# Kernel optimization log

Measured on AMD Instinct MI355X. Metric: run time of the kernel, lower is better.

The kernel has to match this reference:

```python
import jax, jax.numpy as jnp
import numpy as np

B, N, F, DEG = 64, 1024, 128, 8
K1, K2, K3 = 512, 256, 128  # ceil(0.5*N) cascaded pool sizes
NUM_CLASSES = 10
E = B * N * DEG

def _elu(x):
    return jnp.where(x > 0, x, jnp.expm1(x))

def gcn(x, W, b, src, dst, ev, n):
    # PyG GCNConv with improved=True: self-loop weight 2, symmetric norm
    h = x @ W
    w = ev.astype(h.dtype)
    deg = jax.ops.segment_sum(w, dst, num_segments=n) + 2.0
    dinv = jax.lax.rsqrt(deg)
    coef = (w * dinv[src] * dinv[dst])[:, None]
    out = jax.ops.segment_sum(h[src] * coef, dst, num_segments=n)
    out = out + h * (2.0 * dinv * dinv)[:, None]  # self-loop term
    return out + b

def topk_pool(x, p, src, dst, ev, bg, npg, k):
    # score = tanh(x.p/||p||); keep top-k per graph; mask+remap edges
    score = jnp.tanh((x @ p) / jnp.linalg.norm(p))
    vals, idx = jax.lax.top_k(score.reshape(bg, npg), k)
    perm = (idx + (jnp.arange(bg) * npg)[:, None]).reshape(-1)
    x_new = x[perm] * vals.reshape(-1)[:, None]
    remap = jnp.full((bg * npg,), -1, jnp.int32).at[perm].set(
        jnp.arange(bg * k, dtype=jnp.int32))
    s2, d2 = remap[src], remap[dst]
    ev2 = ev & (s2 >= 0) & (d2 >= 0)
    return x_new, jnp.maximum(s2, 0), jnp.maximum(d2, 0), ev2, perm

def setup_inputs() -> dict:
    key = jax.random.key(0)
    ks = jax.random.split(key, 16)
    offs = (jnp.arange(B) * N)[:, None]
    e_per = DEG * N
    src = (jax.random.randint(ks[0], (B, e_per), 0, N) + offs).reshape(-1).astype(jnp.int32)
    dst = (jax.random.randint(ks[1], (B, e_per), 0, N) + offs).reshape(-1).astype(jnp.int32)
    def w(k, shape, fan_in):
        return jax.random.normal(k, shape, jnp.float32) / np.sqrt(fan_in)
    return {
        "x": jax.random.normal(ks[2], (B * N, F), jnp.float32),
        "W1": w(ks[3], (F, 32), F), "b1": jnp.zeros((32,)), "p1": w(ks[4], (32,), 32),
        "W2": w(ks[5], (32, 64), 32), "b2": jnp.zeros((64,)), "p2": w(ks[6], (64,), 64),
        "W3": w(ks[7], (64, 128), 64), "b3": jnp.zeros((128,)), "p3": w(ks[8], (128,), 128),
        "W4": w(ks[9], (128, 256), 128), "b4": jnp.zeros((256,)),
        "W5": w(ks[10], (384, 128), 384), "b5": jnp.zeros((128,)),
        "W6": w(ks[11], (192, 64), 192), "b6": jnp.zeros((64,)),
        "W7": w(ks[12], (96, 32), 96), "b7": jnp.zeros((32,)),
        "Wl": w(ks[13], (64, 64), 64),
        "Wc": w(ks[14], (64, NUM_CLASSES), 64), "bc": jnp.zeros((NUM_CLASSES,)),
        "src": src, "dst": dst,
    }

def reference(x, W1, b1, p1, W2, b2, p2, W3, b3, p3, W4, b4,
              W5, b5, W6, b6, W7, b7, Wl, Wc, bc, src, dst):
    ev0 = jnp.ones((E,), bool)
    x1 = _elu(gcn(x, W1, b1, src, dst, ev0, B * N))
    x2, s2, d2, ev2, idx2 = topk_pool(x1, p1, src, dst, ev0, B, N, K1)
    x2 = _elu(x2)
    x3 = _elu(gcn(x2, W2, b2, s2, d2, ev2, B * K1))
    x4, s4, d4, ev4, idx4 = topk_pool(x3, p2, s2, d2, ev2, B, K1, K2)
    x4 = _elu(x4)
    x5 = _elu(gcn(x4, W3, b3, s4, d4, ev4, B * K2))
    x6, s6, d6, ev6, idx6 = topk_pool(x5, p3, s4, d4, ev4, B, K2, K3)
    x6 = _elu(x6)
    x7 = _elu(gcn(x6, W4, b4, s6, d6, ev6, B * K3))
    x8 = jnp.zeros((B * K2, 256), x7.dtype).at[idx6].set(x7)
    x8 = _elu(jnp.concatenate([x8, x5], axis=1))
    x9 = _elu(gcn(x8, W5, b5, s4, d4, ev4, B * K2))
    x10 = jnp.zeros((B * K1, 128), x9.dtype).at[idx4].set(x9)
    x10 = _elu(jnp.concatenate([x10, x3], axis=1))
    x11 = _elu(gcn(x10, W6, b6, s2, d2, ev2, B * K1))
    x12 = jnp.zeros((B * N, 64), x11.dtype).at[idx2].set(x11)
    x12 = _elu(jnp.concatenate([x12, x1], axis=1))
    x13 = _elu(gcn(x12, W7, b7, src, dst, ev0, B * N))
    batch = jnp.repeat(jnp.arange(B), N)
    gmp = jax.ops.segment_max(x13, batch, num_segments=B)
    gap = jax.ops.segment_sum(x13, batch, num_segments=B) / N
    g = _elu(jnp.concatenate([gmp, gap], axis=1))
    g = _elu(g @ Wl)
    logits = g @ Wc + bc
    return jax.nn.log_softmax(logits, axis=-1)
```

## Files before the change

kernel.cpp:

```cpp
#include <hip/hip_runtime.h>
#include <hip/hip_bf16.h>
#include <math.h>

#define B_ 64
#define N_ 1024
#define E_ 524288
#define K1_ 512
#define K2_ 256
#define K3_ 128
#define M0_ 65536
#define M1_ 32768
#define M2_ 16384
#define M3_ 8192

static __device__ __forceinline__ float eluf(float x){ return x > 0.f ? x : expm1f(x); }
static __device__ __forceinline__ float4 elu4(float4 v){
  float4 o; o.x=eluf(v.x); o.y=eluf(v.y); o.z=eluf(v.z); o.w=eluf(v.w); return o;
}

template<int BM,int BN,int MODE>
__global__ __launch_bounds__(256) void k_mm(const float* __restrict__ X,
    const float* __restrict__ W, float* __restrict__ H, int M, int K, int N,
    const int* __restrict__ perm, const float* __restrict__ vals,
    const float* __restrict__ Xd, const int* __restrict__ orig,
    const int* __restrict__ rm, int WD4){
  constexpr int TX = BN/4;
  constexpr int TY = 256/TX;
  constexpr int RM = BM/TY;
  __shared__ float Xs[BM][36];
  __shared__ float Ws[32][BN];
  const int t = threadIdx.x;
  const int tx = t % TX, ty = t / TX;
  const int m0 = blockIdx.x*BM, n0 = blockIdx.y*BN;
  float acc[RM][4];
  #pragma unroll
  for (int r=0;r<RM;++r){acc[r][0]=0.f;acc[r][1]=0.f;acc[r][2]=0.f;acc[r][3]=0.f;}
  for (int k0=0;k0<K;k0+=32){
    #pragma unroll
    for (int r=0;r<BM/32;++r){
      int fi=r*256+t, row=fi>>3, q=fi&7;
      int m = m0+row;
      int c4 = (k0>>2)+q;
      float4 v;
      if (MODE==0){
        v = *(const float4*)(X + (size_t)m*K + (c4<<2));
      } else if (MODE==1){
        int pm = perm[m]; float vv = vals[m];
        float4 h = *(const float4*)(X + (size_t)pm*K + (c4<<2));
        v.x=eluf(h.x*vv); v.y=eluf(h.y*vv); v.z=eluf(h.z*vv); v.w=eluf(h.w*vv);
      } else {
        if (c4 < WD4){
          int o = orig ? orig[m] : m;
          int j = rm[o];
          if (j>=0) v = elu4(*(const float4*)(Xd + ((size_t)j*WD4 + c4)*4));
          else { v.x=0.f;v.y=0.f;v.z=0.f;v.w=0.f; }
        } else {
          int ws4 = (K>>2) - WD4;
          v = elu4(*(const float4*)(X + ((size_t)m*ws4 + (c4-WD4))*4));
        }
      }
      *(float4*)(&Xs[row][q*4]) = v;
    }
    #pragma unroll
    for (int r=0;r<BN/32;++r){
      int fi=r*256+t, row=fi/(BN/4), q=fi%(BN/4);
      *(float4*)(&Ws[row][q*4]) = *(const float4*)(W + (size_t)(k0+row)*N + n0 + q*4);
    }
    __syncthreads();
    #pragma unroll
    for (int kk=0;kk<32;++kk){
      float4 wv = *(const float4*)(&Ws[kk][tx*4]);
      #pragma unroll
      for (int r=0;r<RM;++r){
        float xv = Xs[ty*RM+r][kk];
        acc[r][0]=fmaf(xv,wv.x,acc[r][0]);
        acc[r][1]=fmaf(xv,wv.y,acc[r][1]);
        acc[r][2]=fmaf(xv,wv.z,acc[r][2]);
        acc[r][3]=fmaf(xv,wv.w,acc[r][3]);
      }
    }
    __syncthreads();
  }
  #pragma unroll
  for (int r=0;r<RM;++r){
    int m = m0 + ty*RM + r;
    float4 h; h.x=acc[r][0];h.y=acc[r][1];h.z=acc[r][2];h.w=acc[r][3];
    *(float4*)(H + (size_t)m*N + n0 + tx*4) = h;
  }
}

__global__ void k_deg0(const int* __restrict__ dst, int* __restrict__ degi){
  int i = blockIdx.x*256+threadIdx.x; if (i>=E_) return;
  atomicAdd(&degi[dst[i]], 1);
}
__global__ void k_place0(const int* __restrict__ src, const int* __restrict__ dst,
                         int* __restrict__ cursor, int* __restrict__ col){
  int i = blockIdx.x*256+threadIdx.x; if (i>=E_) return;
  int p = atomicAdd(&cursor[dst[i]], 1);
  col[p] = src[i];
}

__global__ __launch_bounds__(256) void k_scanA(const int* __restrict__ degi,
                                               int* __restrict__ bsum){
  __shared__ int ls[256];
  int b = blockIdx.x, t = threadIdx.x;
  ls[t] = degi[b*256+t]; __syncthreads();
  for (int o=128;o>0;o>>=1){ if (t<o) ls[t]+=ls[t+o]; __syncthreads(); }
  if (t==0) bsum[b] = ls[0];
}
__global__ __launch_bounds__(256) void k_scanB(int* __restrict__ bsum){
  __shared__ int ps[256];
  int t = threadIdx.x;
  ps[t] = bsum[t]; __syncthreads();
  for (int o=1;o<256;o<<=1){
    int v = (t>=o) ? ps[t-o] : 0;
    __syncthreads(); ps[t]+=v; __syncthreads();
  }
  bsum[t] = ps[t];
}
__global__ __launch_bounds__(256) void k_scanC(const int* __restrict__ degi,
    const int* __restrict__ bsum, int* __restrict__ rowptr,
    int* __restrict__ cursor, float* __restrict__ dinv){
  __shared__ int ps[256];
  int b = blockIdx.x, t = threadIdx.x;
  int i = b*256+t;
  int d = degi[i];
  ps[t] = d; __syncthreads();
  for (int o=1;o<256;o<<=1){
    int v = (t>=o) ? ps[t-o] : 0;
    __syncthreads(); ps[t]+=v; __syncthreads();
  }
  int off = (b==0 ? 0 : bsum[b-1]) + ps[t] - d;
  rowptr[i] = off; cursor[i] = off;
  dinv[i] = rsqrtf((float)d + 2.f);
  if (i == M0_-1) rowptr[M0_] = off + d;
}

__global__ void k_deg_orig(const int* __restrict__ orig, const int* __restrict__ rowptr0,
                           const int* __restrict__ col0, const int* __restrict__ rm,
                           float* __restrict__ dinv, int M){
  int i = blockIdx.x*256+threadIdx.x; if (i>=M) return;
  int o = orig[i];
  int beg = rowptr0[o], end = rowptr0[o+1];
  int d = 0;
  for (int j=beg;j<end;++j) d += (rm[col0[j]] >= 0) ? 1 : 0;
  dinv[i] = rsqrtf((float)d + 2.f);
}

__global__ void k_compose_idx(const int* __restrict__ prevOrig, const int* __restrict__ idxL,
                              int* __restrict__ origL, int n){
  int i = blockIdx.x*256+threadIdx.x; if (i<n) origL[i] = prevOrig[idxL[i]];
}

template<int F, bool SCORE>
__global__ __launch_bounds__(256) void k_gather(const int* __restrict__ rowptr,
    const int* __restrict__ col, const float* __restrict__ dinv,
    const float* __restrict__ H, const float* __restrict__ bias,
    float* __restrict__ OUT, int M,
    const float* __restrict__ p, float* __restrict__ score){
  constexpr int FQ = F/4;
  int i = blockIdx.x*256+threadIdx.x;
  if (i >= M*FQ) return;
  int n = i/FQ, q = i - (i/FQ)*FQ;
  int beg = rowptr[n], end = rowptr[n+1];
  float4 acc; acc.x=0.f;acc.y=0.f;acc.z=0.f;acc.w=0.f;
  for (int j=beg;j<end;++j){
    int s = col[j];
    float c = dinv[s];
    float4 h = *(const float4*)(H + (size_t)s*F + q*4);
    acc.x=fmaf(c,h.x,acc.x); acc.y=fmaf(c,h.y,acc.y);
    acc.z=fmaf(c,h.z,acc.z); acc.w=fmaf(c,h.w,acc.w);
  }
  float dn = dinv[n];
  float sc = 2.f*dn*dn;
  float4 hn = *(const float4*)(H + (size_t)n*F + q*4);
  float4 bv = *(const float4*)(bias + q*4);
  float4 o;
  o.x = eluf(fmaf(sc,hn.x,fmaf(dn,acc.x,bv.x)));
  o.y = eluf(fmaf(sc,hn.y,fmaf(dn,acc.y,bv.y)));
  o.z = eluf(fmaf(sc,hn.z,fmaf(dn,acc.z,bv.z)));
  o.w = eluf(fmaf(sc,hn.w,fmaf(dn,acc.w,bv.w)));
  *(float4*)(OUT + (size_t)n*F + q*4) = o;
  if (SCORE){
    float4 pv = *(const float4*)(p + q*4);
    float dot = o.x*pv.x + o.y*pv.y + o.z*pv.z + o.w*pv.w;
    float n2  = pv.x*pv.x + pv.y*pv.y + pv.z*pv.z + pv.w*pv.w;
    #pragma unroll
    for (int mk=FQ>>1; mk>0; mk>>=1){
      dot += __shfl_xor(dot, mk);
      n2  += __shfl_xor(n2,  mk);
    }
    if (q==0) score[n] = tanhf(dot * rsqrtf(n2));
  }
}

template<int F, bool SCORE>
__global__ __launch_bounds__(256) void k_gather_rm(const int* __restrict__ orig,
    const int* __restrict__ rowptr0, const int* __restrict__ col0,
    const int* __restrict__ rm, const float* __restrict__ dinv,
    const float* __restrict__ H, const float* __restrict__ bias,
    float* __restrict__ OUT, int M,
    const float* __restrict__ p, float* __restrict__ score){
  constexpr int FQ = F/4;
  int i = blockIdx.x*256+threadIdx.x;
  if (i >= M*FQ) return;
  int n = i/FQ, q = i - (i/FQ)*FQ;
  int o = orig[n];
  int beg = rowptr0[o], end = rowptr0[o+1];
  float4 acc; acc.x=0.f;acc.y=0.f;acc.z=0.f;acc.w=0.f;
  for (int j=beg;j<end;++j){
    int s = rm[col0[j]];
    if (s >= 0){
      float c = dinv[s];
      float4 h = *(const float4*)(H + (size_t)s*F + q*4);
      acc.x=fmaf(c,h.x,acc.x); acc.y=fmaf(c,h.y,acc.y);
      acc.z=fmaf(c,h.z,acc.z); acc.w=fmaf(c,h.w,acc.w);
    }
  }
  float dn = dinv[n];
  float sc = 2.f*dn*dn;
  float4 hn = *(const float4*)(H + (size_t)n*F + q*4);
  float4 bv = *(const float4*)(bias + q*4);
  float4 ov;
  ov.x = eluf(fmaf(sc,hn.x,fmaf(dn,acc.x,bv.x)));
  ov.y = eluf(fmaf(sc,hn.y,fmaf(dn,acc.y,bv.y)));
  ov.z = eluf(fmaf(sc,hn.z,fmaf(dn,acc.z,bv.z)));
  ov.w = eluf(fmaf(sc,hn.w,fmaf(dn,acc.w,bv.w)));
  *(float4*)(OUT + (size_t)n*F + q*4) = ov;
  if (SCORE){
    float4 pv = *(const float4*)(p + q*4);
    float dot = ov.x*pv.x + ov.y*pv.y + ov.z*pv.z + ov.w*pv.w;
    float n2  = pv.x*pv.x + pv.y*pv.y + pv.z*pv.z + pv.w*pv.w;
    #pragma unroll
    for (int mk=FQ>>1; mk>0; mk>>=1){
      dot += __shfl_xor(dot, mk);
      n2  += __shfl_xor(n2,  mk);
    }
    if (q==0) score[n] = tanhf(dot * rsqrtf(n2));
  }
}

__global__ void k_topk(const float* __restrict__ score, int npg, int K,
                       int* __restrict__ perm, float* __restrict__ vals){
  __shared__ float ss[1024]; __shared__ int si[1024];
  int g = blockIdx.x, tid = threadIdx.x;
  ss[tid] = score[g*npg + tid]; si[tid] = tid;
  __syncthreads();
  for (int k=2;k<=npg;k<<=1){
    for (int j=k>>1;j>0;j>>=1){
      int ixj = tid ^ j;
      if (ixj > tid){
        float s1=ss[tid], s2=ss[ixj]; int i1=si[tid], i2=si[ixj];
        bool aAfterB = (s1 < s2) || (s1==s2 && i1 > i2);
        bool sw = ((tid & k)==0) ? aAfterB : !aAfterB;
        if (sw){ ss[tid]=s2; si[tid]=i2; ss[ixj]=s1; si[ixj]=i1; }
      }
      __syncthreads();
    }
  }
  if (tid < K){ perm[g*K+tid] = g*npg + si[tid]; vals[g*K+tid] = ss[tid]; }
}

__global__ void k_remap_set(const int* __restrict__ perm, int* __restrict__ remap, int n){
  int i = blockIdx.x*256+threadIdx.x; if (i<n) remap[perm[i]] = i;
}

__global__ void k_head(const float* __restrict__ x13, const float* __restrict__ Wl,
                       const float* __restrict__ Wc, const float* __restrict__ bc,
                       float* __restrict__ out){
  __shared__ float smax[256], ssum[256];
  __shared__ float gv[64], g2[64], logit[10];
  int g = blockIdx.x, t = threadIdx.x;
  int f = t & 31, r0 = t >> 5;
  float mx = -3.4e38f, sm = 0.f;
  const float* base = x13 + (size_t)g*N_*32;
  for (int r=r0; r<N_; r+=8){ float v = base[r*32+f]; mx = fmaxf(mx,v); sm += v; }
  smax[t]=mx; ssum[t]=sm; __syncthreads();
  if (t<128){ smax[t]=fmaxf(smax[t],smax[t+128]); ssum[t]+=ssum[t+128]; } __syncthreads();
  if (t<64){ smax[t]=fmaxf(smax[t],smax[t+64]); ssum[t]+=ssum[t+64]; } __syncthreads();
  if (t<32){
    float m2 = fmaxf(smax[t],smax[t+32]); float s2 = ssum[t]+ssum[t+32];
    gv[t] = eluf(m2); gv[32+t] = eluf(s2 * (1.f/N_));
  }
  __syncthreads();
  if (t<64){
    float acc=0.f;
    #pragma unroll
    for (int i2=0;i2<64;++i2) acc = fmaf(gv[i2], Wl[i2*64+t], acc);
    g2[t] = eluf(acc);
  }
  __syncthreads();
  if (t<10){
    float acc = bc[t];
    #pragma unroll
    for (int j=0;j<64;++j) acc = fmaf(g2[j], Wc[j*10+t], acc);
    logit[t] = acc;
  }
  __syncthreads();
  if (t==0){
    float m=-3.4e38f; for (int c=0;c<10;++c) m=fmaxf(m,logit[c]);
    float s=0.f; for (int c=0;c<10;++c) s += expf(logit[c]-m);
    float lse = m + logf(s);
    for (int c=0;c<10;++c) out[g*10+c] = logit[c]-lse;
  }
}

extern "C" void kernel_launch(void* const* d_in, const int* in_sizes, int n_in,
                              void* d_out, int out_size, void* d_ws, size_t ws_size,
                              hipStream_t stream){
  const float* x  = (const float*)d_in[0];
  const float* W1 = (const float*)d_in[1];
  const float* b1 = (const float*)d_in[2];
  const float* p1 = (const float*)d_in[3];
  const float* W2 = (const float*)d_in[4];
  const float* b2 = (const float*)d_in[5];
  const float* p2 = (const float*)d_in[6];
  const float* W3 = (const float*)d_in[7];
  const float* b3 = (const float*)d_in[8];
  const float* p3 = (const float*)d_in[9];
  const float* W4 = (const float*)d_in[10];
  const float* b4 = (const float*)d_in[11];
  const float* W5 = (const float*)d_in[12];
  const float* b5 = (const float*)d_in[13];
  const float* W6 = (const float*)d_in[14];
  const float* b6 = (const float*)d_in[15];
  const float* W7 = (const float*)d_in[16];
  const float* b7 = (const float*)d_in[17];
  const float* Wl = (const float*)d_in[18];
  const float* Wc = (const float*)d_in[19];
  const float* bc = (const float*)d_in[20];
  const int* src0 = (const int*)d_in[21];
  const int* dst0 = (const int*)d_in[22];
  float* out = (float*)d_out;

  char* wsp = (char*)d_ws;
  size_t off = 0;
  auto alloc = [&](size_t bytes)->char*{
    char* p = wsp + off;
    off += (bytes + 255) & ~(size_t)255;
    return p;
  };
  float* bufA = (float*)alloc((size_t)2097152*4);
  float* bufB = (float*)alloc((size_t)2097152*4);
  float* bufC = (float*)alloc((size_t)2097152*4);
  float* bufD = (float*)alloc((size_t)2097152*4);
  float* bufH = (float*)alloc((size_t)2097152*4);
  float* score= (float*)alloc((size_t)M0_*4);
  float* vals2= (float*)alloc((size_t)M1_*4);
  float* vals4= (float*)alloc((size_t)M2_*4);
  float* vals6= (float*)alloc((size_t)M3_*4);
  int* idx2 = (int*)alloc((size_t)M1_*4);
  int* idx4 = (int*)alloc((size_t)M2_*4);
  int* idx6 = (int*)alloc((size_t)M3_*4);
  int* orig4 = (int*)alloc((size_t)M2_*4);
  int* orig6 = (int*)alloc((size_t)M3_*4);
  int* rm02 = (int*)alloc((size_t)M0_*4);
  int* rm04 = (int*)alloc((size_t)M0_*4);
  int* rm06 = (int*)alloc((size_t)M0_*4);
  int* col0 = (int*)alloc((size_t)E_*4);
  int* rowptr0 = (int*)alloc((size_t)(M0_+1)*4);
  int* cursor0 = (int*)alloc((size_t)M0_*4);
  int* degi0 = (int*)alloc((size_t)M0_*4);
  int* bsum  = (int*)alloc((size_t)256*4);
  float* dinv0 = (float*)alloc((size_t)M0_*4);
  float* dinv2 = (float*)alloc((size_t)M1_*4);
  float* dinv4 = (float*)alloc((size_t)M2_*4);
  float* dinv6 = (float*)alloc((size_t)M3_*4);

  auto NB = [](int total){ return (total+255)/256; };

  hipMemsetAsync(degi0, 0, (size_t)M0_*4, stream);
  k_deg0<<<NB(E_),256,0,stream>>>(dst0, degi0);
  k_scanA<<<256,256,0,stream>>>(degi0, bsum);
  k_scanB<<<1,256,0,stream>>>(bsum);
  k_scanC<<<256,256,0,stream>>>(degi0, bsum, rowptr0, cursor0, dinv0);
  k_place0<<<NB(E_),256,0,stream>>>(src0, dst0, cursor0, col0);

  k_mm<64,32,0><<<dim3(M0_/64,1),256,0,stream>>>(x, W1, bufH, M0_, 128, 32,
      nullptr,nullptr,nullptr,nullptr,nullptr,0);
  k_gather<32,true><<<NB(M0_*8),256,0,stream>>>(rowptr0, col0, dinv0, bufH, b1, bufA, M0_, p1, score);

  k_topk<<<B_,1024,0,stream>>>(score, 1024, K1_, idx2, vals2);
  hipMemsetAsync(rm02, 0xFF, (size_t)M0_*4, stream);
  k_remap_set<<<NB(M1_),256,0,stream>>>(idx2, rm02, M1_);
  k_deg_orig<<<NB(M1_),256,0,stream>>>(idx2, rowptr0, col0, rm02, dinv2, M1_);

  k_mm<64,64,1><<<dim3(M1_/64,1),256,0,stream>>>(bufA, W2, bufH, M1_, 32, 64,
      idx2, vals2, nullptr,nullptr,nullptr,0);
  k_gather_rm<64,true><<<NB(M1_*16),256,0,stream>>>(idx2, rowptr0, col0, rm02, dinv2, bufH, b2, bufB, M1_, p2, score);

  k_topk<<<B_,512,0,stream>>>(score, 512, K2_, idx4, vals4);
  k_compose_idx<<<NB(M2_),256,0,stream>>>(idx2, idx4, orig4, M2_);
  hipMemsetAsync(rm04, 0xFF, (size_t)M0_*4, stream);
  k_remap_set<<<NB(M2_),256,0,stream>>>(orig4, rm04, M2_);
  k_deg_orig<<<NB(M2_),256,0,stream>>>(orig4, rowptr0, col0, rm04, dinv4, M2_);

  k_mm<64,64,1><<<dim3(M2_/64,2),256,0,stream>>>(bufB, W3, bufH, M2_, 64, 128,
      idx4, vals4, nullptr,nullptr,nullptr,0);
  k_gather_rm<128,true><<<NB(M2_*32),256,0,stream>>>(orig4, rowptr0, col0, rm04, dinv4, bufH, b3, bufC, M2_, p3, score);

  k_topk<<<B_,256,0,stream>>>(score, 256, K3_, idx6, vals6);
  k_compose_idx<<<NB(M3_),256,0,stream>>>(orig4, idx6, orig6, M3_);
  hipMemsetAsync(rm06, 0xFF, (size_t)M0_*4, stream);
  k_remap_set<<<NB(M3_),256,0,stream>>>(orig6, rm06, M3_);
  k_deg_orig<<<NB(M3_),256,0,stream>>>(orig6, rowptr0, col0, rm06, dinv6, M3_);

  k_mm<64,64,1><<<dim3(M3_/64,4),256,0,stream>>>(bufC, W4, bufH, M3_, 128, 256,
      idx6, vals6, nullptr,nullptr,nullptr,0);
  k_gather_rm<256,false><<<NB(M3_*64),256,0,stream>>>(orig6, rowptr0, col0, rm06, dinv6, bufH, b4, bufD, M3_, nullptr, nullptr);

  k_mm<64,64,2><<<dim3(M2_/64,2),256,0,stream>>>(bufC, W5, bufH, M2_, 384, 128,
      nullptr,nullptr, bufD, orig4, rm06, 64);
  k_gather_rm<128,false><<<NB(M2_*32),256,0,stream>>>(orig4, rowptr0, col0, rm04, dinv4, bufH, b5, bufD, M2_, nullptr, nullptr);

  k_mm<64,64,2><<<dim3(M1_/64,1),256,0,stream>>>(bufB, W6, bufH, M1_, 192, 64,
      nullptr,nullptr, bufD, idx2, rm04, 32);
  k_gather_rm<64,false><<<NB(M1_*16),256,0,stream>>>(idx2, rowptr0, col0, rm02, dinv2, bufH, b6, bufC, M1_, nullptr, nullptr);

  k_mm<64,32,2><<<dim3(M0_/64,1),256,0,stream>>>(bufA, W7, bufH, M0_, 96, 32,
      nullptr,nullptr, bufC, nullptr, rm02, 16);
  k_gather<32,false><<<NB(M0_*8),256,0,stream>>>(rowptr0, col0, dinv0, bufH, b7, bufA, M0_, nullptr, nullptr);

  k_head<<<B_,256,0,stream>>>(bufA, Wl, Wc, bc, out);

  (void)in_sizes; (void)n_in; (void)out_size; (void)ws_size;
}
```

Before: 399.9 us.

## Prefetch next GEMM tile into registers and transpose X tile in shared memory

The tiled GEMM now loads the next K-slice of X and W into registers while computing on the current shared-memory tile, overlapping global loads with FMAs. The X tile is stored transposed in shared memory, so each thread reads its four rows with a single float4 load and the inner loop is hand-unrolled for exactly four rows. The two BN=32 launches move to BM=128 so that every instantiation has four rows per thread. This adds register pressure and relies on RM always being 4, and the transposed scalar stores into shared memory may cause bank conflicts.

After: 416.0 us. 4.0% more time.

```diff
diff --git a/kernel.cpp b/kernel.cpp
--- a/kernel.cpp
+++ b/kernel.cpp
@@ -27,18 +27,23 @@
   constexpr int TX = BN/4;
   constexpr int TY = 256/TX;
   constexpr int RM = BM/TY;
-  __shared__ float Xs[BM][36];
+  constexpr int XLD = BM/32;
+  constexpr int WLD = BN/32;
+  constexpr int XST = BM+4;
+  __shared__ float Xs[32][XST];
   __shared__ float Ws[32][BN];
   const int t = threadIdx.x;
   const int tx = t % TX, ty = t / TX;
   const int m0 = blockIdx.x*BM, n0 = blockIdx.y*BN;
+  float4 xr[XLD], wr[WLD];
   float acc[RM][4];
   #pragma unroll
   for (int r=0;r<RM;++r){acc[r][0]=0.f;acc[r][1]=0.f;acc[r][2]=0.f;acc[r][3]=0.f;}
-  for (int k0=0;k0<K;k0+=32){
-    #pragma unroll
-    for (int r=0;r<BM/32;++r){
-      int fi=r*256+t, row=fi>>3, q=fi&7;
+
+  auto load_step = [&](int k0){
+    #pragma unroll
+    for (int l=0;l<XLD;++l){
+      int fi=l*256+t, row=fi>>3, q=fi&7;
       int m = m0+row;
       int c4 = (k0>>2)+q;
       float4 v;
@@ -59,25 +64,42 @@
           v = elu4(*(const float4*)(X + ((size_t)m*ws4 + (c4-WD4))*4));
         }
       }
-      *(float4*)(&Xs[row][q*4]) = v;
-    }
-    #pragma unroll
-    for (int r=0;r<BN/32;++r){
-      int fi=r*256+t, row=fi/(BN/4), q=fi%(BN/4);
-      *(float4*)(&Ws[row][q*4]) = *(const float4*)(W + (size_t)(k0+row)*N + n0 + q*4);
+      xr[l]=v;
+    }
+    #pragma unroll
+    for (int l=0;l<WLD;++l){
+      int fi=l*256+t, wrow=fi/(BN/4), wq=fi%(BN/4);
+      wr[l] = *(const float4*)(W + (size_t)(k0+wrow)*N + n0 + wq*4);
+    }
+  };
+
+  load_step(0);
+  for (int k0=0;k0<K;k0+=32){
+    #pragma unroll
+    for (int l=0;l<XLD;++l){
+      int fi=l*256+t, row=fi>>3, q=fi&7;
+      Xs[q*4+0][row]=xr[l].x; Xs[q*4+1][row]=xr[l].y;
+      Xs[q*4+2][row]=xr[l].z; Xs[q*4+3][row]=xr[l].w;
+    }
+    #pragma unroll
+    for (int l=0;l<WLD;++l){
+      int fi=l*256+t, wrow=fi/(BN/4), wq=fi%(BN/4);
+      *(float4*)(&Ws[wrow][wq*4]) = wr[l];
     }
     __syncthreads();
+    if (k0+32 < K) load_step(k0+32);
     #pragma unroll
     for (int kk=0;kk<32;++kk){
       float4 wv = *(const float4*)(&Ws[kk][tx*4]);
-      #pragma unroll
-      for (int r=0;r<RM;++r){
-        float xv = Xs[ty*RM+r][kk];
-        acc[r][0]=fmaf(xv,wv.x,acc[r][0]);
-        acc[r][1]=fmaf(xv,wv.y,acc[r][1]);
-        acc[r][2]=fmaf(xv,wv.z,acc[r][2]);
-        acc[r][3]=fmaf(xv,wv.w,acc[r][3]);
-      }
+      float4 xv = *(const float4*)(&Xs[kk][ty*RM]);
+      acc[0][0]=fmaf(xv.x,wv.x,acc[0][0]); acc[0][1]=fmaf(xv.x,wv.y,acc[0][1]);
+      acc[0][2]=fmaf(xv.x,wv.z,acc[0][2]); acc[0][3]=fmaf(xv.x,wv.w,acc[0][3]);
+      acc[1][0]=fmaf(xv.y,wv.x,acc[1][0]); acc[1][1]=fmaf(xv.y,wv.y,acc[1][1]);
+      acc[1][2]=fmaf(xv.y,wv.z,acc[1][2]); acc[1][3]=fmaf(xv.y,wv.w,acc[1][3]);
+      acc[2][0]=fmaf(xv.z,wv.x,acc[2][0]); acc[2][1]=fmaf(xv.z,wv.y,acc[2][1]);
+      acc[2][2]=fmaf(xv.z,wv.z,acc[2][2]); acc[2][3]=fmaf(xv.z,wv.w,acc[2][3]);
+      acc[3][0]=fmaf(xv.w,wv.x,acc[3][0]); acc[3][1]=fmaf(xv.w,wv.y,acc[3][1]);
+      acc[3][2]=fmaf(xv.w,wv.z,acc[3][2]); acc[3][3]=fmaf(xv.w,wv.w,acc[3][3]);
     }
     __syncthreads();
   }
@@ -376,7 +398,7 @@
   k_scanC<<<256,256,0,stream>>>(degi0, bsum, rowptr0, cursor0, dinv0);
   k_place0<<<NB(E_),256,0,stream>>>(src0, dst0, cursor0, col0);
 
-  k_mm<64,32,0><<<dim3(M0_/64,1),256,0,stream>>>(x, W1, bufH, M0_, 128, 32,
+  k_mm<128,32,0><<<dim3(M0_/128,1),256,0,stream>>>(x, W1, bufH, M0_, 128, 32,
       nullptr,nullptr,nullptr,nullptr,nullptr,0);
   k_gather<32,true><<<NB(M0_*8),256,0,stream>>>(rowptr0, col0, dinv0, bufH, b1, bufA, M0_, p1, score);
 
@@ -417,7 +439,7 @@
       nullptr,nullptr, bufD, idx2, rm04, 32);
   k_gather_rm<64,false><<<NB(M1_*16),256,0,stream>>>(idx2, rowptr0, col0, rm02, dinv2, bufH, b6, bufC, M1_, nullptr, nullptr);
 
-  k_mm<64,32,2><<<dim3(M0_/64,1),256,0,stream>>>(bufA, W7, bufH, M0_, 96, 32,
+  k_mm<128,32,2><<<dim3(M0_/128,1),256,0,stream>>>(bufA, W7, bufH, M0_, 96, 32,
       nullptr,nullptr, bufC, nullptr, rm02, 16);
   k_gather<32,false><<<NB(M0_*8),256,0,stream>>>(rowptr0, col0, dinv0, bufH, b7, bufA, M0_, nullptr, nullptr);
 
```

## Replace tiled fused-gather matmul with row-per-thread matmul plus separate gather/concat kernels

Applied to the files above, without the earlier changes.

Replaces the shared-memory tiled k_mm, which fused the pooling gather, ELU and concat into its X load, with a row-per-thread kernel. Each 64-thread block stages a 32-column weight slice in shared memory and every thread streams its own input row with float4 loads. The gathers and concatenations move into separate k_pool_gather4 and k_cat kernels that write contiguous staging buffers. The W5 matmul is split over K into two halves that k_add4 then sums. This adds extra kernel launches and global round trips for the staged inputs. Per-thread row loads are strided across lanes, so global coalescing is poor.

New measurement: 459.9 us. 1.15x slower.

```diff
diff --git a/kernel.cpp b/kernel.cpp
--- a/kernel.cpp
+++ b/kernel.cpp
@@ -18,75 +18,56 @@
   float4 o; o.x=eluf(v.x); o.y=eluf(v.y); o.z=eluf(v.z); o.w=eluf(v.w); return o;
 }
 
-template<int BM,int BN,int MODE>
-__global__ __launch_bounds__(256) void k_mm(const float* __restrict__ X,
-    const float* __restrict__ W, float* __restrict__ H, int M, int K, int N,
-    const int* __restrict__ perm, const float* __restrict__ vals,
-    const float* __restrict__ Xd, const int* __restrict__ orig,
-    const int* __restrict__ rm, int WD4){
-  constexpr int TX = BN/4;
-  constexpr int TY = 256/TX;
-  constexpr int RM = BM/TY;
-  __shared__ float Xs[BM][36];
-  __shared__ float Ws[32][BN];
+template<int KZ>
+__global__ __launch_bounds__(64) void k_mmrs(const float* __restrict__ X,
+    const float* __restrict__ W, float* __restrict__ H, int M, int K, int N){
+  __shared__ float Ws[KZ*32];
   const int t = threadIdx.x;
-  const int tx = t % TX, ty = t / TX;
-  const int m0 = blockIdx.x*BM, n0 = blockIdx.y*BN;
-  float acc[RM][4];
+  const int row = blockIdx.x*64 + t;
+  const int n0 = blockIdx.y*32;
+  const int kb = blockIdx.z*KZ;
+  float4* Ws4 = (float4*)Ws;
   #pragma unroll
-  for (int r=0;r<RM;++r){acc[r][0]=0.f;acc[r][1]=0.f;acc[r][2]=0.f;acc[r][3]=0.f;}
-  for (int k0=0;k0<K;k0+=32){
+  for (int l=0; l<KZ*8/64; ++l){
+    int fi = l*64 + t;
+    int k = fi>>3, c4 = fi&7;
+    Ws4[fi] = *(const float4*)(W + (size_t)(kb+k)*N + n0 + c4*4);
+  }
+  __syncthreads();
+  const float* xr = X + (size_t)row*K + kb;
+  float4 a[8];
+  #pragma unroll
+  for (int c=0;c<8;++c){a[c].x=0.f;a[c].y=0.f;a[c].z=0.f;a[c].w=0.f;}
+  float4 xv = *(const float4*)(xr);
+  for (int k4=0; k4<KZ/4; ++k4){
+    float4 xn = xv;
+    if (k4+1 < KZ/4) xn = *(const float4*)(xr + (k4+1)*4);
+    const float4* wrow = Ws4 + k4*32;
     #pragma unroll
-    for (int r=0;r<BM/32;++r){
-      int fi=r*256+t, row=fi>>3, q=fi&7;
-      int m = m0+row;
-      int c4 = (k0>>2)+q;
-      float4 v;
-      if (MODE==0){
-        v = *(const float4*)(X + (size_t)m*K + (c4<<2));
-      } else if (MODE==1){
-        int pm = perm[m]; float vv = vals[m];
-        float4 h = *(const float4*)(X + (size_t)pm*K + (c4<<2));
-        v.x=eluf(h.x*vv); v.y=eluf(h.y*vv); v.z=eluf(h.z*vv); v.w=eluf(h.w*vv);
-      } else {
-        if (c4 < WD4){
-          int o = orig ? orig[m] : m;
-          int j = rm[o];
-          if (j>=0) v = elu4(*(const float4*)(Xd + ((size_t)j*WD4 + c4)*4));
-          else { v.x=0.f;v.y=0.f;v.z=0.f;v.w=0.f; }
-        } else {
-          int ws4 = (K>>2) - WD4;
-          v = elu4(*(const float4*)(X + ((size_t)m*ws4 + (c4-WD4))*4));
-        }
-      }
-      *(float4*)(&Xs[row][q*4]) = v;
-    }
-    #pragma unroll
-    for (int r=0;r<BN/32;++r){
-      int fi=r*256+t, row=fi/(BN/4), q=fi%(BN/4);
-      *(float4*)(&Ws[row][q*4]) = *(const float4*)(W + (size_t)(k0+row)*N + n0 + q*4);
-    }
-    __syncthreads();
-    #pragma unroll
-    for (int kk=0;kk<32;++kk){
-      float4 wv = *(const float4*)(&Ws[kk][tx*4]);
+    for (int j=0;j<4;++j){
+      float xk = (j==0)?xv.x:(j==1)?xv.y:(j==2)?xv.z:xv.w;
       #pragma unroll
-      for (int r=0;r<RM;++r){
-        float xv = Xs[ty*RM+r][kk];
-        acc[r][0]=fmaf(xv,wv.x,acc[r][0]);
-        acc[r][1]=fmaf(xv,wv.y,acc[r][1]);
-        acc[r][2]=fmaf(xv,wv.z,acc[r][2]);
-        acc[r][3]=fmaf(xv,wv.w,acc[r][3]);
+      for (int c=0;c<8;++c){
+        float4 w = wrow[j*8+c];
+        a[c].x = fmaf(xk,w.x,a[c].x);
+        a[c].y = fmaf(xk,w.y,a[c].y);
+        a[c].z = fmaf(xk,w.z,a[c].z);
+        a[c].w = fmaf(xk,w.w,a[c].w);
       }
     }
-    __syncthreads();
-  }
+    xv = xn;
+  }
+  float* hr = H + (size_t)blockIdx.z*M*N + (size_t)row*N + n0;
   #pragma unroll
-  for (int r=0;r<RM;++r){
-    int m = m0 + ty*RM + r;
-    float4 h; h.x=acc[r][0];h.y=acc[r][1];h.z=acc[r][2];h.w=acc[r][3];
-    *(float4*)(H + (size_t)m*N + n0 + tx*4) = h;
-  }
+  for (int c=0;c<8;++c) *(float4*)(hr + c*4) = a[c];
+}
+
+__global__ void k_add4(float* __restrict__ a, const float* __restrict__ b, int n4){
+  int i = blockIdx.x*256+threadIdx.x; if (i>=n4) return;
+  float4 x = ((float4*)a)[i];
+  float4 y = ((const float4*)b)[i];
+  x.x+=y.x; x.y+=y.y; x.z+=y.z; x.w+=y.w;
+  ((float4*)a)[i]=x;
 }
 
 __global__ void k_deg0(const int* __restrict__ dst, int* __restrict__ degi){
@@ -263,6 +244,39 @@
 
 __global__ void k_remap_set(const int* __restrict__ perm, int* __restrict__ remap, int n){
   int i = blockIdx.x*256+threadIdx.x; if (i<n) remap[perm[i]] = i;
+}
+
+__global__ void k_pool_gather4(const float* __restrict__ Xin, const int* __restrict__ perm,
+                               const float* __restrict__ vals, float* __restrict__ Xout,
+                               int Mout, int fqsh, int fsh){
+  int total = Mout<<fqsh;
+  int i = blockIdx.x*256+threadIdx.x; if (i>=total) return;
+  int m = i>>fqsh, q = i&((1<<fqsh)-1);
+  float v = vals[m];
+  float4 h = *(const float4*)(Xin + ((size_t)perm[m]<<fsh) + q*4);
+  float4 o; o.x=eluf(h.x*v); o.y=eluf(h.y*v); o.z=eluf(h.z*v); o.w=eluf(h.w*v);
+  *(float4*)(Xout + ((size_t)m<<fsh) + q*4) = o;
+}
+
+template<int WD4,int WS4>
+__global__ void k_cat(const float* __restrict__ Xd, const int* __restrict__ orig,
+                      const int* __restrict__ rm, const float* __restrict__ Xs,
+                      float* __restrict__ cat, int rows){
+  constexpr int W4 = WD4+WS4;
+  int total = rows*W4;
+  int i = blockIdx.x*256+threadIdx.x; if (i>=total) return;
+  int r = i/W4, c = i - r*W4;
+  float4 v;
+  if (c < WD4){
+    int o = orig ? orig[r] : r;
+    int j = rm[o];
+    if (j>=0) v = *(const float4*)(Xd + (size_t)j*(WD4*4) + c*4);
+    else { v.x=0.f;v.y=0.f;v.z=0.f;v.w=0.f; }
+  } else {
+    v = *(const float4*)(Xs + (size_t)r*(WS4*4) + (c-WD4)*4);
+  }
+  float4 o4; o4.x=eluf(v.x); o4.y=eluf(v.y); o4.z=eluf(v.z); o4.w=eluf(v.w);
+  *(float4*)(cat + (size_t)i*4) = o4;
 }
 
 __global__ void k_head(const float* __restrict__ x13, const float* __restrict__ Wl,
@@ -344,7 +358,9 @@
   float* bufB = (float*)alloc((size_t)2097152*4);
   float* bufC = (float*)alloc((size_t)2097152*4);
   float* bufD = (float*)alloc((size_t)2097152*4);
-  float* bufH = (float*)alloc((size_t)2097152*4);
+  float* bufH = (float*)alloc((size_t)4194304*4);
+  float* cat  = (float*)alloc((size_t)6291456*4);
+  float* s1   = (float*)alloc((size_t)1048576*4);
   float* score= (float*)alloc((size_t)M0_*4);
   float* vals2= (float*)alloc((size_t)M1_*4);
   float* vals4= (float*)alloc((size_t)M2_*4);
@@ -376,17 +392,16 @@
   k_scanC<<<256,256,0,stream>>>(degi0, bsum, rowptr0, cursor0, dinv0);
   k_place0<<<NB(E_),256,0,stream>>>(src0, dst0, cursor0, col0);
 
-  k_mm<64,32,0><<<dim3(M0_/64,1),256,0,stream>>>(x, W1, bufH, M0_, 128, 32,
-      nullptr,nullptr,nullptr,nullptr,nullptr,0);
+  k_mmrs<128><<<dim3(M0_/64,1,1),64,0,stream>>>(x, W1, bufH, M0_, 128, 32);
   k_gather<32,true><<<NB(M0_*8),256,0,stream>>>(rowptr0, col0, dinv0, bufH, b1, bufA, M0_, p1, score);
 
   k_topk<<<B_,1024,0,stream>>>(score, 1024, K1_, idx2, vals2);
   hipMemsetAsync(rm02, 0xFF, (size_t)M0_*4, stream);
   k_remap_set<<<NB(M1_),256,0,stream>>>(idx2, rm02, M1_);
   k_deg_orig<<<NB(M1_),256,0,stream>>>(idx2, rowptr0, col0, rm02, dinv2, M1_);
-
-  k_mm<64,64,1><<<dim3(M1_/64,1),256,0,stream>>>(bufA, W2, bufH, M1_, 32, 64,
-      idx2, vals2, nullptr,nullptr,nullptr,0);
+  k_pool_gather4<<<NB(M1_*8),256,0,stream>>>(bufA, idx2, vals2, s1, M1_, 3, 5);
+
+  k_mmrs<32><<<dim3(M1_/64,2,1),64,0,stream>>>(s1, W2, bufH, M1_, 32, 64);
   k_gather_rm<64,true><<<NB(M1_*16),256,0,stream>>>(idx2, rowptr0, col0, rm02, dinv2, bufH, b2, bufB, M1_, p2, score);
 
   k_topk<<<B_,512,0,stream>>>(score, 512, K2_, idx4, vals4);
@@ -394,9 +409,9 @@
   hipMemsetAsync(rm04, 0xFF, (size_t)M0_*4, stream);
   k_remap_set<<<NB(M2_),256,0,stream>>>(orig4, rm04, M2_);
   k_deg_orig<<<NB(M2_),256,0,stream>>>(orig4, rowptr0, col0, rm04, dinv4, M2_);
-
-  k_mm<64,64,1><<<dim3(M2_/64,2),256,0,stream>>>(bufB, W3, bufH, M2_, 64, 128,
-      idx4, vals4, nullptr,nullptr,nullptr,0);
+  k_pool_gather4<<<NB(M2_*16),256,0,stream>>>(bufB, idx4, vals4, s1, M2_, 4, 6);
+
+  k_mmrs<64><<<dim3(M2_/64,4,1),64,0,stream>>>(s1, W3, bufH, M2_, 64, 128);
   k_gather_rm<128,true><<<NB(M2_*32),256,0,stream>>>(orig4, rowptr0, col0, rm04, dinv4, bufH, b3, bufC, M2_, p3, score);
 
   k_topk<<<B_,256,0,stream>>>(score, 256, K3_, idx6, vals6);
@@ -404,21 +419,22 @@
   hipMemsetAsync(rm06, 0xFF, (size_t)M0_*4, stream);
   k_remap_set<<<NB(M3_),256,0,stream>>>(orig6, rm06, M3_);
   k_deg_orig<<<NB(M3_),256,0,stream>>>(orig6, rowptr0, col0, rm06, dinv6, M3_);
-
-  k_mm<64,64,1><<<dim3(M3_/64,4),256,0,stream>>>(bufC, W4, bufH, M3_, 128, 256,
-      idx6, vals6, nullptr,nullptr,nullptr,0);
+  k_pool_gather4<<<NB(M3_*32),256,0,stream>>>(bufC, idx6, vals6, s1, M3_, 5, 7);
+
+  k_mmrs<128><<<dim3(M3_/64,8,1),64,0,stream>>>(s1, W4, bufH, M3_, 128, 256);
   k_gather_rm<256,false><<<NB(M3_*64),256,0,stream>>>(orig6, rowptr0, col0, rm06, dinv6, bufH, b4, bufD, M3_, nullptr, nullptr);
 
-  k_mm<64,64,2><<<dim3(M2_/64,2),256,0,stream>>>(bufC, W5, bufH, M2_, 384, 128,
-      nullptr,nullptr, bufD, orig4, rm06, 64);
+  k_cat<64,32><<<NB(M2_*96),256,0,stream>>>(bufD, orig4, rm06, bufC, cat, M2_);
+  k_mmrs<192><<<dim3(M2_/64,4,2),64,0,stream>>>(cat, W5, bufH, M2_, 384, 128);
+  k_add4<<<NB(M2_*32),256,0,stream>>>(bufH, bufH + (size_t)M2_*128, M2_*32);
   k_gather_rm<128,false><<<NB(M2_*32),256,0,stream>>>(orig4, rowptr0, col0, rm04, dinv4, bufH, b5, bufD, M2_, nullptr, nullptr);
 
-  k_mm<64,64,2><<<dim3(M1_/64,1),256,0,stream>>>(bufB, W6, bufH, M1_, 192, 64,
-      nullptr,nullptr, bufD, idx2, rm04, 32);
+  k_cat<32,16><<<NB(M1_*48),256,0,stream>>>(bufD, idx2, rm04, bufB, cat, M1_);
+  k_mmrs<192><<<dim3(M1_/64,2,1),64,0,stream>>>(cat, W6, bufH, M1_, 192, 64);
   k_gather_rm<64,false><<<NB(M1_*16),256,0,stream>>>(idx2, rowptr0, col0, rm02, dinv2, bufH, b6, bufC, M1_, nullptr, nullptr);
 
-  k_mm<64,32,2><<<dim3(M0_/64,1),256,0,stream>>>(bufA, W7, bufH, M0_, 96, 32,
-      nullptr,nullptr, bufC, nullptr, rm02, 16);
+  k_cat<16,8><<<NB(M0_*24),256,0,stream>>>(bufC, nullptr, rm02, bufA, cat, M0_);
+  k_mmrs<96><<<dim3(M0_/64,1,1),64,0,stream>>>(cat, W7, bufH, M0_, 96, 32);
   k_gather<32,false><<<NB(M0_*8),256,0,stream>>>(rowptr0, col0, dinv0, bufH, b7, bufA, M0_, nullptr, nullptr);
 
   k_head<<<B_,256,0,stream>>>(bufA, Wl, Wc, bc, out);
```
